# Performance work log

Hardware: AMD Instinct MI355X
Metric: run time of the kernel (lower is better)

The kernel has to match this reference:

```python
import jax, jax.numpy as jnp
import numpy as np

INFINITY = 1000000000000.0
HEADS = 12
HEAD_SIZE = 64


def setup_inputs() -> dict:
    key = jax.random.key(0)
    k1, k2 = jax.random.split(key)
    B, S, H = 8, 512, 1024
    x = jax.random.normal(k1, (B, S, H), dtype=jnp.float32)
    mask = jnp.ones((B, S), dtype=jnp.float32)
    W = jax.random.normal(k2, (H, HEADS * HEAD_SIZE * 2), dtype=jnp.float32) * (1.0 / np.sqrt(H))
    b = jnp.zeros((HEADS * HEAD_SIZE * 2,), dtype=jnp.float32)
    return {"x": x, "mask": mask, "W": W, "b": b}


def _sinusoidal_pos(seq_len, dim, dtype):
    # pos[n, d] interleaved as [sin0, cos0, sin1, cos1, ...]
    position = jnp.arange(seq_len, dtype=dtype)  # (S,)
    indices = jnp.power(jnp.asarray(10000.0, dtype), -2.0 * jnp.arange(dim // 2, dtype=dtype) / dim)
    ang = position[:, None] * indices[None, :]  # (S, d/2)
    pos = jnp.stack([jnp.sin(ang), jnp.cos(ang)], axis=-1).reshape(seq_len, dim)
    return pos


def reference(x, mask, W, b):
    B, S, _ = x.shape
    hs = HEAD_SIZE
    proj = x @ W + b  # (B, S, HEADS*2*hs)
    proj = proj.reshape(B, S, HEADS, 2 * hs)
    qw, kw = proj[..., :hs], proj[..., hs:]  # (B, S, HEADS, hs)

    # RoPE (note: original uses torch .repeat, i.e. TILING, not interleave)
    pos = _sinusoidal_pos(S, hs, x.dtype)  # (S, hs)
    cos_half = pos[None, :, None, 1::2]  # (1, S, 1, hs/2)
    sin_half = pos[None, :, None, ::2]
    cos_pos = jnp.concatenate([cos_half, cos_half], axis=-1)  # tiled -> (1,S,1,hs)
    sin_pos = jnp.concatenate([sin_half, sin_half], axis=-1)

    def rotate(t):
        t2 = jnp.stack([-t[..., 1::2], t[..., ::2]], axis=-1).reshape(t.shape)
        return t * cos_pos + t2 * sin_pos

    qw = rotate(qw)
    kw = rotate(kw)

    logits = jnp.einsum('bmhd,bnhd->bhmn', qw, kw)  # (B, HEADS, S, S)

    # sequence masking on dim 2 (rows) and dim 3 (cols)
    m_row = mask[:, None, :, None]
    m_col = mask[:, None, None, :]
    logits = logits * m_row + (-INFINITY) * (1.0 - m_row)
    logits = logits * m_col + (-INFINITY) * (1.0 - m_col)

    # strictly-lower-triangular mask (exclude end < start)
    tri = jnp.tril(jnp.ones((S, S), dtype=logits.dtype), k=-1)
    logits = logits - tri * INFINITY
    return logits / (hs ** 0.5)
```

## Files before the change

### kernel.cpp

```cpp
#include <hip/hip_runtime.h>
#include <stdint.h>
#include <stddef.h>

#define SS 512
#define HID 1024
#define NHEADS 12
#define HSZ 64
#define NPROJ 1536
#define NEG_INF 1000000000000.0f

typedef __attribute__((ext_vector_type(4))) float f32x4;
typedef __attribute__((ext_vector_type(8))) __bf16 bf16x8;
typedef __attribute__((ext_vector_type(4))) unsigned short us4;

typedef __attribute__((address_space(1))) unsigned char gu8;
typedef __attribute__((address_space(3))) unsigned char lu8;

static __device__ __forceinline__ void gld16(const void* g, void* l) {
  __builtin_amdgcn_global_load_lds((gu8*)(g), (lu8*)(l), 16, 0, 0);
}

static __device__ __forceinline__ unsigned short f2bf(float f) {
  union { float f; unsigned u; } x; x.f = f;
  unsigned r = x.u + 0x7fffu + ((x.u >> 16) & 1u);
  return (unsigned short)(r >> 16);
}

__global__ __launch_bounds__(256) void k_prep(
    const float4* __restrict__ x, const float* __restrict__ W,
    float2* __restrict__ tab, us4* __restrict__ xb, unsigned short* __restrict__ wbt) {
  __shared__ float t[32][33];
  const int bid = blockIdx.x;
  const int tid = threadIdx.x;
  if (bid < 64) {
    int tt = bid * 256 + tid;
    int s = tt >> 5, i = tt & 31;
    float rate = powf(10000.0f, -(float)i / 32.0f);
    float sv, cv;
    sincosf((float)s * rate, &sv, &cv);
    tab[tt] = make_float2(sv, cv);
  } else if (bid < 64 + 4096) {
    int i = (bid - 64) * 256 + tid;
    float4 v = x[i];
    us4 o;
    o[0] = f2bf(v.x); o[1] = f2bf(v.y); o[2] = f2bf(v.z); o[3] = f2bf(v.w);
    xb[i] = o;
  } else {
    int flat = bid - (64 + 4096);
    int n0 = (flat % 48) * 32, k0 = (flat / 48) * 32;
    int tx = tid & 31, ty = tid >> 5;
#pragma unroll
    for (int i = 0; i < 4; ++i)
      t[ty + i * 8][tx] = W[(k0 + ty + i * 8) * NPROJ + n0 + tx];
    __syncthreads();
#pragma unroll
    for (int i = 0; i < 4; ++i)
      wbt[(n0 + ty + i * 8) * HID + (k0 + tx)] = f2bf(t[tx][ty + i * 8]);
  }
}

__global__ __launch_bounds__(256) void k_proj(
    const unsigned short* __restrict__ xb, const unsigned short* __restrict__ wbt,
    const float* __restrict__ bias, const float2* __restrict__ tab,
    unsigned short* __restrict__ qo, unsigned short* __restrict__ ko) {
  __shared__ __align__(16) unsigned short lA[2][128 * 64];
  __shared__ __align__(16) unsigned short lB[2][96 * 64];
  const int tid = threadIdx.x;
  const int lane = tid & 63, w = tid >> 6;
  const int wm = w >> 1, wn = w & 1;
  const int m0 = blockIdx.x * 128, n0 = blockIdx.y * 96;

  const char* aptr[4]; const char* bptr[3];
  int adst[4], bdst[3];
#pragma unroll
  for (int c = 0; c < 4; ++c) {
    int lin = (w * 4 + c) * 1024 + lane * 16;
    int row = lin >> 7, cb = lin & 127;
    aptr[c] = (const char*)(xb + (size_t)(m0 + row) * HID) + (cb ^ ((row & 7) << 4));
    adst[c] = (w * 4 + c) * 1024;
  }
#pragma unroll
  for (int c = 0; c < 3; ++c) {
    int lin = (w * 3 + c) * 1024 + lane * 16;
    int row = lin >> 7, cb = lin & 127;
    bptr[c] = (const char*)(wbt + (size_t)(n0 + row) * HID) + (cb ^ ((row & 7) << 4));
    bdst[c] = (w * 3 + c) * 1024;
  }

  f32x4 acc[3][4];
#pragma unroll
  for (int a = 0; a < 3; ++a)
#pragma unroll
    for (int b = 0; b < 4; ++b)
      acc[a][b] = (f32x4)(0.0f);

#define STAGE(buf, kt)                                                      \
  do {                                                                      \
    _Pragma("unroll") for (int c = 0; c < 4; ++c)                           \
        gld16(aptr[c] + (kt) * 128, (char*)(&lA[(buf)][0]) + adst[c]);      \
    _Pragma("unroll") for (int c = 0; c < 3; ++c)                           \
        gld16(bptr[c] + (kt) * 128, (char*)(&lB[(buf)][0]) + bdst[c]);      \
  } while (0)

  __builtin_amdgcn_sched_barrier(0);
  STAGE(0, 0);

  for (int kt = 0; kt < 16; ++kt) {
    const int cur = kt & 1;
    if (kt < 15) {
      STAGE(cur ^ 1, kt + 1);
      asm volatile("s_waitcnt vmcnt(7)" ::: "memory");
    } else {
      asm volatile("s_waitcnt vmcnt(0)" ::: "memory");
    }
    __builtin_amdgcn_s_barrier();
#pragma unroll
    for (int ks = 0; ks < 2; ++ks) {
      bf16x8 af[3], bf[4];
      const int kb = ks * 64 + (lane >> 4) * 16;
#pragma unroll
      for (int a = 0; a < 3; ++a) {
        int row = wn * 48 + a * 16 + (lane & 15);
        af[a] = *(const bf16x8*)((const char*)(&lB[cur][0]) + row * 128 + (kb ^ ((row & 7) << 4)));
      }
#pragma unroll
      for (int b = 0; b < 4; ++b) {
        int row = wm * 64 + b * 16 + (lane & 15);
        bf[b] = *(const bf16x8*)((const char*)(&lA[cur][0]) + row * 128 + (kb ^ ((row & 7) << 4)));
      }
#pragma unroll
      for (int a = 0; a < 3; ++a)
#pragma unroll
        for (int b = 0; b < 4; ++b)
          acc[a][b] = __builtin_amdgcn_mfma_f32_16x16x32_bf16(af[a], bf[b], acc[a][b], 0, 0, 0);
    }
    asm volatile("s_waitcnt lgkmcnt(0)" ::: "memory");
    __builtin_amdgcn_s_barrier();
  }
#undef STAGE
  __builtin_amdgcn_sched_barrier(0);

#pragma unroll
  for (int a = 0; a < 3; ++a) {
    const int nq = n0 + wn * 48 + a * 16 + (lane >> 4) * 4;
    const float4 bv = *(const float4*)(bias + nq);
    const int d = nq & 63;
    const int h = nq >> 7;
    unsigned short* base = ((nq >> 6) & 1) ? ko : qo;
#pragma unroll
    for (int b = 0; b < 4; ++b) {
      const int mrow = m0 + wm * 64 + b * 16 + (lane & 15);
      const int s = mrow & (SS - 1);
      const int bidx = mrow >> 9;
      const float2* tp = tab + s * 32 + (d & 31);
      const float4 ta = *(const float4*)(tp);
      const float4 tb = *(const float4*)(tp + 2);
      float v0 = acc[a][b][0] + bv.x;
      float v1 = acc[a][b][1] + bv.y;
      float v2 = acc[a][b][2] + bv.z;
      float v3 = acc[a][b][3] + bv.w;
      float o0 = v0 * ta.y - v1 * ta.x;
      float o1 = v1 * ta.w + v0 * ta.z;
      float o2 = v2 * tb.y - v3 * tb.x;
      float o3 = v3 * tb.w + v2 * tb.z;
      us4 pk;
      pk[0] = f2bf(o0); pk[1] = f2bf(o1); pk[2] = f2bf(o2); pk[3] = f2bf(o3);
      *(us4*)(base + ((size_t)(bidx * NHEADS + h) * SS + s) * HSZ + d) = pk;
    }
  }
}

__global__ __launch_bounds__(256) void k_logits(
    const unsigned short* __restrict__ q, const unsigned short* __restrict__ kk,
    const float* __restrict__ mask, float* __restrict__ out) {
  const int tid = threadIdx.x;
  const int lane = tid & 63, w = tid >> 6;
  const int bh = blockIdx.y;
  const int b = bh / NHEADS;
  const int m0 = (blockIdx.x >> 2) * 128, n0 = (blockIdx.x & 3) * 128;
  const char* qbase = (const char*)(q + (size_t)bh * SS * HSZ);
  const char* kbase = (const char*)(kk + (size_t)bh * SS * HSZ);

  int mrow[4], nrow[4];
#pragma unroll
  for (int i = 0; i < 4; ++i) {
    mrow[i] = m0 + (w >> 1) * 64 + i * 16 + (lane & 15);
    nrow[i] = n0 + (w & 1) * 64 + i * 16 + (lane & 15);
  }

  f32x4 acc[4][4];
#pragma unroll
  for (int a = 0; a < 4; ++a)
#pragma unroll
    for (int bb = 0; bb < 4; ++bb)
      acc[a][bb] = (f32x4)(0.0f);

#pragma unroll
  for (int ks = 0; ks < 2; ++ks) {
    const int kboff = ks * 64 + (lane >> 4) * 16;
    bf16x8 kf[4], qf[4];
#pragma unroll
    for (int i = 0; i < 4; ++i)
      kf[i] = *(const bf16x8*)(kbase + (size_t)nrow[i] * 128 + kboff);
#pragma unroll
    for (int i = 0; i < 4; ++i)
      qf[i] = *(const bf16x8*)(qbase + (size_t)mrow[i] * 128 + kboff);
#pragma unroll
    for (int ni = 0; ni < 4; ++ni)
#pragma unroll
      for (int mi = 0; mi < 4; ++mi)
        acc[ni][mi] = __builtin_amdgcn_mfma_f32_16x16x32_bf16(kf[ni], qf[mi], acc[ni][mi], 0, 0, 0);
  }

#pragma unroll
  for (int mi = 0; mi < 4; ++mi) {
    const int m = mrow[mi];
    const float mr = mask[b * SS + m];
    float* orow = out + ((size_t)bh * SS + m) * SS;
#pragma unroll
    for (int ni = 0; ni < 4; ++ni) {
      const int nb = n0 + (w & 1) * 64 + ni * 16 + (lane >> 4) * 4;
      const float4 mc = *(const float4*)(mask + b * SS + nb);
      f32x4 res;
#pragma unroll
      for (int r = 0; r < 4; ++r) {
        float v = acc[ni][mi][r];
        const float mcv = (r == 0) ? mc.x : (r == 1) ? mc.y : (r == 2) ? mc.z : mc.w;
        v = v * mr - NEG_INF * (1.0f - mr);
        v = v * mcv - NEG_INF * (1.0f - mcv);
        if (m > nb + r) v -= NEG_INF;
        res[r] = v * 0.125f;
      }
      *(f32x4*)(orow + nb) = res;
    }
  }
}

extern "C" void kernel_launch(void* const* d_in, const int* in_sizes, int n_in,
                              void* d_out, int out_size, void* d_ws, size_t ws_size,
                              hipStream_t stream) {
  const float* x = (const float*)d_in[0];
  const float* mask = (const float*)d_in[1];
  const float* W = (const float*)d_in[2];
  const float* bias = (const float*)d_in[3];
  float* out = (float*)d_out;

  char* ws = (char*)d_ws;
  float2* tab = (float2*)ws;
  unsigned short* xb = (unsigned short*)(ws + 131072);
  unsigned short* wbt = (unsigned short*)(ws + 131072 + 8388608);
  unsigned short* qo = (unsigned short*)(ws + 131072 + 8388608 + 3145728);
  unsigned short* ko = (unsigned short*)(ws + 131072 + 8388608 + 3145728 + 6291456);

  k_prep<<<dim3(64 + 4096 + 1536), dim3(256), 0, stream>>>(
      (const float4*)x, W, tab, (us4*)xb, wbt);
  k_proj<<<dim3(32, 16), dim3(256), 0, stream>>>(xb, wbt, bias, tab, qo, ko);
  k_logits<<<dim3(16, 96), dim3(256), 0, stream>>>(qo, ko, mask, out);
}
```

Baseline: 59.26 us.

## Fuse prep, projection and logits into one persistent kernel with grid barriers

Merges the three kernels into a single persistent kernel of 512 blocks that loops over the prep, projection and logits work, with atomic-counter grid barriers between phases. This removes two kernel launch boundaries and the drain/ramp gaps between them. In exchange it adds a memset launch, spin-wait barriers, and the risk of deadlock if all 512 blocks are not co-resident (launch bounds request two blocks per CU). Logits work now runs as three iterations per block instead of a wide grid.

After: 181.4 us. 3.06x slower.

```diff
diff --git a/kernel.cpp b/kernel.cpp
--- a/kernel.cpp
+++ b/kernel.cpp
@@ -8,6 +8,7 @@
 #define HSZ 64
 #define NPROJ 1536
 #define NEG_INF 1000000000000.0f
+#define GRID 512
 
 typedef __attribute__((ext_vector_type(4))) float f32x4;
 typedef __attribute__((ext_vector_type(8))) __bf16 bf16x8;
@@ -26,73 +27,95 @@
   return (unsigned short)(r >> 16);
 }
 
-__global__ __launch_bounds__(256) void k_prep(
-    const float4* __restrict__ x, const float* __restrict__ W,
-    float2* __restrict__ tab, us4* __restrict__ xb, unsigned short* __restrict__ wbt) {
-  __shared__ float t[32][33];
+static __device__ __forceinline__ void gbar(unsigned int* cnt) {
+  __syncthreads();
+  if (threadIdx.x == 0) {
+    __threadfence();
+    __hip_atomic_fetch_add(cnt, 1u, __ATOMIC_RELEASE, __HIP_MEMORY_SCOPE_AGENT);
+    while (__hip_atomic_load(cnt, __ATOMIC_RELAXED, __HIP_MEMORY_SCOPE_AGENT) < GRID)
+      __builtin_amdgcn_s_sleep(2);
+    __threadfence();
+  }
+  __syncthreads();
+}
+
+__global__ __launch_bounds__(256, 2) void k_fused(
+    const float4* __restrict__ x, const float* __restrict__ Wg,
+    const float* __restrict__ mask, const float* __restrict__ bias,
+    float2* __restrict__ tab, us4* __restrict__ xb4,
+    unsigned short* __restrict__ wbt,
+    unsigned short* __restrict__ qo, unsigned short* __restrict__ ko,
+    float* __restrict__ out, unsigned int* __restrict__ barcnt) {
+  __shared__ __align__(16) unsigned short smem[2 * 8192 + 2 * 6144];
   const int bid = blockIdx.x;
   const int tid = threadIdx.x;
-  if (bid < 64) {
-    int tt = bid * 256 + tid;
-    int s = tt >> 5, i = tt & 31;
-    float rate = powf(10000.0f, -(float)i / 32.0f);
-    float sv, cv;
-    sincosf((float)s * rate, &sv, &cv);
-    tab[tt] = make_float2(sv, cv);
-  } else if (bid < 64 + 4096) {
-    int i = (bid - 64) * 256 + tid;
-    float4 v = x[i];
-    us4 o;
-    o[0] = f2bf(v.x); o[1] = f2bf(v.y); o[2] = f2bf(v.z); o[3] = f2bf(v.w);
-    xb[i] = o;
-  } else {
-    int flat = bid - (64 + 4096);
-    int n0 = (flat % 48) * 32, k0 = (flat / 48) * 32;
-    int tx = tid & 31, ty = tid >> 5;
-#pragma unroll
-    for (int i = 0; i < 4; ++i)
-      t[ty + i * 8][tx] = W[(k0 + ty + i * 8) * NPROJ + n0 + tx];
-    __syncthreads();
-#pragma unroll
-    for (int i = 0; i < 4; ++i)
-      wbt[(n0 + ty + i * 8) * HID + (k0 + tx)] = f2bf(t[tx][ty + i * 8]);
-  }
-}
-
-__global__ __launch_bounds__(256) void k_proj(
-    const unsigned short* __restrict__ xb, const unsigned short* __restrict__ wbt,
-    const float* __restrict__ bias, const float2* __restrict__ tab,
-    unsigned short* __restrict__ qo, unsigned short* __restrict__ ko) {
-  __shared__ __align__(16) unsigned short lA[2][128 * 64];
-  __shared__ __align__(16) unsigned short lB[2][96 * 64];
-  const int tid = threadIdx.x;
   const int lane = tid & 63, w = tid >> 6;
-  const int wm = w >> 1, wn = w & 1;
-  const int m0 = blockIdx.x * 128, n0 = blockIdx.y * 96;
-
-  const char* aptr[4]; const char* bptr[3];
-  int adst[4], bdst[3];
-#pragma unroll
-  for (int c = 0; c < 4; ++c) {
-    int lin = (w * 4 + c) * 1024 + lane * 16;
-    int row = lin >> 7, cb = lin & 127;
-    aptr[c] = (const char*)(xb + (size_t)(m0 + row) * HID) + (cb ^ ((row & 7) << 4));
-    adst[c] = (w * 4 + c) * 1024;
-  }
-#pragma unroll
-  for (int c = 0; c < 3; ++c) {
-    int lin = (w * 3 + c) * 1024 + lane * 16;
-    int row = lin >> 7, cb = lin & 127;
-    bptr[c] = (const char*)(wbt + (size_t)(n0 + row) * HID) + (cb ^ ((row & 7) << 4));
-    bdst[c] = (w * 3 + c) * 1024;
-  }
-
-  f32x4 acc[3][4];
-#pragma unroll
-  for (int a = 0; a < 3; ++a)
-#pragma unroll
-    for (int b = 0; b < 4; ++b)
-      acc[a][b] = (f32x4)(0.0f);
+
+  {
+    float(*t)[33] = (float(*)[33])smem;
+    const unsigned short* xb2 = (const unsigned short*)xb4;
+    (void)xb2;
+    for (int u = bid; u < 64 + 4096 + 1536; u += GRID) {
+      if (u < 64) {
+        int tt = u * 256 + tid;
+        int s = tt >> 5, i = tt & 31;
+        float rate = powf(10000.0f, -(float)i / 32.0f);
+        float sv, cv;
+        sincosf((float)s * rate, &sv, &cv);
+        tab[tt] = make_float2(sv, cv);
+      } else if (u < 64 + 4096) {
+        int i = (u - 64) * 256 + tid;
+        float4 v = x[i];
+        us4 o;
+        o[0] = f2bf(v.x); o[1] = f2bf(v.y); o[2] = f2bf(v.z); o[3] = f2bf(v.w);
+        xb4[i] = o;
+      } else {
+        int flat = u - (64 + 4096);
+        int n0 = (flat % 48) * 32, k0 = (flat / 48) * 32;
+        int tx = tid & 31, ty = tid >> 5;
+#pragma unroll
+        for (int i = 0; i < 4; ++i)
+          t[ty + i * 8][tx] = Wg[(k0 + ty + i * 8) * NPROJ + n0 + tx];
+        __syncthreads();
+#pragma unroll
+        for (int i = 0; i < 4; ++i)
+          wbt[(n0 + ty + i * 8) * HID + (k0 + tx)] = f2bf(t[tx][ty + i * 8]);
+        __syncthreads();
+      }
+    }
+  }
+  gbar(barcnt + 0);
+
+  {
+    const unsigned short* xb = (const unsigned short*)xb4;
+    unsigned short(*lA)[8192] = (unsigned short(*)[8192])smem;
+    unsigned short(*lB)[6144] = (unsigned short(*)[6144])(smem + 16384);
+    const int wm = w >> 1, wn = w & 1;
+    const int m0 = (bid & 31) * 128, n0 = (bid >> 5) * 96;
+
+    const char* aptr[4]; const char* bptr[3];
+    int adst[4], bdst[3];
+#pragma unroll
+    for (int c = 0; c < 4; ++c) {
+      int lin = (w * 4 + c) * 1024 + lane * 16;
+      int row = lin >> 7, cb = lin & 127;
+      aptr[c] = (const char*)(xb + (size_t)(m0 + row) * HID) + (cb ^ ((row & 7) << 4));
+      adst[c] = (w * 4 + c) * 1024;
+    }
+#pragma unroll
+    for (int c = 0; c < 3; ++c) {
+      int lin = (w * 3 + c) * 1024 + lane * 16;
+      int row = lin >> 7, cb = lin & 127;
+      bptr[c] = (const char*)(wbt + (size_t)(n0 + row) * HID) + (cb ^ ((row & 7) << 4));
+      bdst[c] = (w * 3 + c) * 1024;
+    }
+
+    f32x4 acc[3][4];
+#pragma unroll
+    for (int a = 0; a < 3; ++a)
+#pragma unroll
+      for (int b = 0; b < 4; ++b)
+        acc[a][b] = (f32x4)(0.0f);
 
 #define STAGE(buf, kt)                                                      \
   do {                                                                      \
@@ -102,136 +125,135 @@
         gld16(bptr[c] + (kt) * 128, (char*)(&lB[(buf)][0]) + bdst[c]);      \
   } while (0)
 
-  __builtin_amdgcn_sched_barrier(0);
-  STAGE(0, 0);
-
-  for (int kt = 0; kt < 16; ++kt) {
-    const int cur = kt & 1;
-    if (kt < 15) {
-      STAGE(cur ^ 1, kt + 1);
-      asm volatile("s_waitcnt vmcnt(7)" ::: "memory");
-    } else {
-      asm volatile("s_waitcnt vmcnt(0)" ::: "memory");
-    }
-    __builtin_amdgcn_s_barrier();
+    __builtin_amdgcn_sched_barrier(0);
+    STAGE(0, 0);
+
+    for (int kt = 0; kt < 16; ++kt) {
+      const int cur = kt & 1;
+      if (kt < 15) {
+        STAGE(cur ^ 1, kt + 1);
+        asm volatile("s_waitcnt vmcnt(7)" ::: "memory");
+      } else {
+        asm volatile("s_waitcnt vmcnt(0)" ::: "memory");
+      }
+      __builtin_amdgcn_s_barrier();
+#pragma unroll
+      for (int ks = 0; ks < 2; ++ks) {
+        bf16x8 af[3], bf[4];
+        const int kb = ks * 64 + (lane >> 4) * 16;
+#pragma unroll
+        for (int a = 0; a < 3; ++a) {
+          int row = wn * 48 + a * 16 + (lane & 15);
+          af[a] = *(const bf16x8*)((const char*)(&lB[cur][0]) + row * 128 + (kb ^ ((row & 7) << 4)));
+        }
+#pragma unroll
+        for (int b = 0; b < 4; ++b) {
+          int row = wm * 64 + b * 16 + (lane & 15);
+          bf[b] = *(const bf16x8*)((const char*)(&lA[cur][0]) + row * 128 + (kb ^ ((row & 7) << 4)));
+        }
+#pragma unroll
+        for (int a = 0; a < 3; ++a)
+#pragma unroll
+          for (int b = 0; b < 4; ++b)
+            acc[a][b] = __builtin_amdgcn_mfma_f32_16x16x32_bf16(af[a], bf[b], acc[a][b], 0, 0, 0);
+      }
+      asm volatile("s_waitcnt lgkmcnt(0)" ::: "memory");
+      __builtin_amdgcn_s_barrier();
+    }
+#undef STAGE
+    __builtin_amdgcn_sched_barrier(0);
+
+#pragma unroll
+    for (int a = 0; a < 3; ++a) {
+      const int nq = n0 + wn * 48 + a * 16 + (lane >> 4) * 4;
+      const float4 bv = *(const float4*)(bias + nq);
+      const int d = nq & 63;
+      const int h = nq >> 7;
+      unsigned short* base = ((nq >> 6) & 1) ? ko : qo;
+#pragma unroll
+      for (int b = 0; b < 4; ++b) {
+        const int mrow = m0 + wm * 64 + b * 16 + (lane & 15);
+        const int s = mrow & (SS - 1);
+        const int bidx = mrow >> 9;
+        const float2* tp = tab + s * 32 + (d & 31);
+        const float4 ta = *(const float4*)(tp);
+        const float4 tb = *(const float4*)(tp + 2);
+        float v0 = acc[a][b][0] + bv.x;
+        float v1 = acc[a][b][1] + bv.y;
+        float v2 = acc[a][b][2] + bv.z;
+        float v3 = acc[a][b][3] + bv.w;
+        float o0 = v0 * ta.y - v1 * ta.x;
+        float o1 = v1 * ta.w + v0 * ta.z;
+        float o2 = v2 * tb.y - v3 * tb.x;
+        float o3 = v3 * tb.w + v2 * tb.z;
+        us4 pk;
+        pk[0] = f2bf(o0); pk[1] = f2bf(o1); pk[2] = f2bf(o2); pk[3] = f2bf(o3);
+        *(us4*)(base + ((size_t)(bidx * NHEADS + h) * SS + s) * HSZ + d) = pk;
+      }
+    }
+  }
+  gbar(barcnt + 1);
+
+  for (int tt = bid; tt < 1536; tt += GRID) {
+    const int bx = tt & 15;
+    const int bh = tt >> 4;
+    const int b = bh / NHEADS;
+    const int m0 = (bx >> 2) * 128, n0 = (bx & 3) * 128;
+    const char* qbase = (const char*)(qo + (size_t)bh * SS * HSZ);
+    const char* kbase = (const char*)(ko + (size_t)bh * SS * HSZ);
+
+    int mrow[4], nrow[4];
+#pragma unroll
+    for (int i = 0; i < 4; ++i) {
+      mrow[i] = m0 + (w >> 1) * 64 + i * 16 + (lane & 15);
+      nrow[i] = n0 + (w & 1) * 64 + i * 16 + (lane & 15);
+    }
+
+    f32x4 acc[4][4];
+#pragma unroll
+    for (int a = 0; a < 4; ++a)
+#pragma unroll
+      for (int bb = 0; bb < 4; ++bb)
+        acc[a][bb] = (f32x4)(0.0f);
+
 #pragma unroll
     for (int ks = 0; ks < 2; ++ks) {
-      bf16x8 af[3], bf[4];
-      const int kb = ks * 64 + (lane >> 4) * 16;
-#pragma unroll
-      for (int a = 0; a < 3; ++a) {
-        int row = wn * 48 + a * 16 + (lane & 15);
-        af[a] = *(const bf16x8*)((const char*)(&lB[cur][0]) + row * 128 + (kb ^ ((row & 7) << 4)));
-      }
-#pragma unroll
-      for (int b = 0; b < 4; ++b) {
-        int row = wm * 64 + b * 16 + (lane & 15);
-        bf[b] = *(const bf16x8*)((const char*)(&lA[cur][0]) + row * 128 + (kb ^ ((row & 7) << 4)));
-      }
-#pragma unroll
-      for (int a = 0; a < 3; ++a)
-#pragma unroll
-        for (int b = 0; b < 4; ++b)
-          acc[a][b] = __builtin_amdgcn_mfma_f32_16x16x32_bf16(af[a], bf[b], acc[a][b], 0, 0, 0);
-    }
-    asm volatile("s_waitcnt lgkmcnt(0)" ::: "memory");
-    __builtin_amdgcn_s_barrier();
-  }
-#undef STAGE
-  __builtin_amdgcn_sched_barrier(0);
-
-#pragma unroll
-  for (int a = 0; a < 3; ++a) {
-    const int nq = n0 + wn * 48 + a * 16 + (lane >> 4) * 4;
-    const float4 bv = *(const float4*)(bias + nq);
-    const int d = nq & 63;
-    const int h = nq >> 7;
-    unsigned short* base = ((nq >> 6) & 1) ? ko : qo;
-#pragma unroll
-    for (int b = 0; b < 4; ++b) {
-      const int mrow = m0 + wm * 64 + b * 16 + (lane & 15);
-      const int s = mrow & (SS - 1);
-      const int bidx = mrow >> 9;
-      const float2* tp = tab + s * 32 + (d & 31);
-      const float4 ta = *(const float4*)(tp);
-      const float4 tb = *(const float4*)(tp + 2);
-      float v0 = acc[a][b][0] + bv.x;
-      float v1 = acc[a][b][1] + bv.y;
-      float v2 = acc[a][b][2] + bv.z;
-      float v3 = acc[a][b][3] + bv.w;
-      float o0 = v0 * ta.y - v1 * ta.x;
-      float o1 = v1 * ta.w + v0 * ta.z;
-      float o2 = v2 * tb.y - v3 * tb.x;
-      float o3 = v3 * tb.w + v2 * tb.z;
-      us4 pk;
-      pk[0] = f2bf(o0); pk[1] = f2bf(o1); pk[2] = f2bf(o2); pk[3] = f2bf(o3);
-      *(us4*)(base + ((size_t)(bidx * NHEADS + h) * SS + s) * HSZ + d) = pk;
-    }
-  }
-}
-
-__global__ __launch_bounds__(256) void k_logits(
-    const unsigned short* __restrict__ q, const unsigned short* __restrict__ kk,
-    const float* __restrict__ mask, float* __restrict__ out) {
-  const int tid = threadIdx.x;
-  const int lane = tid & 63, w = tid >> 6;
-  const int bh = blockIdx.y;
-  const int b = bh / NHEADS;
-  const int m0 = (blockIdx.x >> 2) * 128, n0 = (blockIdx.x & 3) * 128;
-  const char* qbase = (const char*)(q + (size_t)bh * SS * HSZ);
-  const char* kbase = (const char*)(kk + (size_t)bh * SS * HSZ);
-
-  int mrow[4], nrow[4];
-#pragma unroll
-  for (int i = 0; i < 4; ++i) {
-    mrow[i] = m0 + (w >> 1) * 64 + i * 16 + (lane & 15);
-    nrow[i] = n0 + (w & 1) * 64 + i * 16 + (lane & 15);
-  }
-
-  f32x4 acc[4][4];
-#pragma unroll
-  for (int a = 0; a < 4; ++a)
-#pragma unroll
-    for (int bb = 0; bb < 4; ++bb)
-      acc[a][bb] = (f32x4)(0.0f);
-
-#pragma unroll
-  for (int ks = 0; ks < 2; ++ks) {
-    const int kboff = ks * 64 + (lane >> 4) * 16;
-    bf16x8 kf[4], qf[4];
-#pragma unroll
-    for (int i = 0; i < 4; ++i)
-      kf[i] = *(const bf16x8*)(kbase + (size_t)nrow[i] * 128 + kboff);
-#pragma unroll
-    for (int i = 0; i < 4; ++i)
-      qf[i] = *(const bf16x8*)(qbase + (size_t)mrow[i] * 128 + kboff);
-#pragma unroll
-    for (int ni = 0; ni < 4; ++ni)
-#pragma unroll
-      for (int mi = 0; mi < 4; ++mi)
-        acc[ni][mi] = __builtin_amdgcn_mfma_f32_16x16x32_bf16(kf[ni], qf[mi], acc[ni][mi], 0, 0, 0);
-  }
-
-#pragma unroll
-  for (int mi = 0; mi < 4; ++mi) {
-    const int m = mrow[mi];
-    const float mr = mask[b * SS + m];
-    float* orow = out + ((size_t)bh * SS + m) * SS;
-#pragma unroll
-    for (int ni = 0; ni < 4; ++ni) {
-      const int nb = n0 + (w & 1) * 64 + ni * 16 + (lane >> 4) * 4;
-      const float4 mc = *(const float4*)(mask + b * SS + nb);
-      f32x4 res;
-#pragma unroll
-      for (int r = 0; r < 4; ++r) {
-        float v = acc[ni][mi][r];
-        const float mcv = (r == 0) ? mc.x : (r == 1) ? mc.y : (r == 2) ? mc.z : mc.w;
-        v = v * mr - NEG_INF * (1.0f - mr);
-        v = v * mcv - NEG_INF * (1.0f - mcv);
-        if (m > nb + r) v -= NEG_INF;
-        res[r] = v * 0.125f;
-      }
-      *(f32x4*)(orow + nb) = res;
+      const int kboff = ks * 64 + (lane >> 4) * 16;
+      bf16x8 kf[4], qf[4];
+#pragma unroll
+      for (int i = 0; i < 4; ++i)
+        kf[i] = *(const bf16x8*)(kbase + (size_t)nrow[i] * 128 + kboff);
+#pragma unroll
+      for (int i = 0; i < 4; ++i)
+        qf[i] = *(const bf16x8*)(qbase + (size_t)mrow[i] * 128 + kboff);
+#pragma unroll
+      for (int ni = 0; ni < 4; ++ni)
+#pragma unroll
+        for (int mi = 0; mi < 4; ++mi)
+          acc[ni][mi] = __builtin_amdgcn_mfma_f32_16x16x32_bf16(kf[ni], qf[mi], acc[ni][mi], 0, 0, 0);
+    }
+
+#pragma unroll
+    for (int mi = 0; mi < 4; ++mi) {
+      const int m = mrow[mi];
+      const float mr = mask[b * SS + m];
+      float* orow = out + ((size_t)bh * SS + m) * SS;
+#pragma unroll
+      for (int ni = 0; ni < 4; ++ni) {
+        const int nb = n0 + (w & 1) * 64 + ni * 16 + (lane >> 4) * 4;
+        const float4 mc = *(const float4*)(mask + b * SS + nb);
+        f32x4 res;
+#pragma unroll
+        for (int r = 0; r < 4; ++r) {
+          float v = acc[ni][mi][r];
+          const float mcv = (r == 0) ? mc.x : (r == 1) ? mc.y : (r == 2) ? mc.z : mc.w;
+          v = v * mr - NEG_INF * (1.0f - mr);
+          v = v * mcv - NEG_INF * (1.0f - mcv);
+          if (m > nb + r) v -= NEG_INF;
+          res[r] = v * 0.125f;
+        }
+        *(f32x4*)(orow + nb) = res;
+      }
     }
   }
 }
@@ -251,9 +273,9 @@
   unsigned short* wbt = (unsigned short*)(ws + 131072 + 8388608);
   unsigned short* qo = (unsigned short*)(ws + 131072 + 8388608 + 3145728);
   unsigned short* ko = (unsigned short*)(ws + 131072 + 8388608 + 3145728 + 6291456);
-
-  k_prep<<<dim3(64 + 4096 + 1536), dim3(256), 0, stream>>>(
-      (const float4*)x, W, tab, (us4*)xb, wbt);
-  k_proj<<<dim3(32, 16), dim3(256), 0, stream>>>(xb, wbt, bias, tab, qo, ko);
-  k_logits<<<dim3(16, 96), dim3(256), 0, stream>>>(qo, ko, mask, out);
-}
+  unsigned int* barcnt = (unsigned int*)(ws + 32 * 1024 * 1024);
+
+  hipMemsetAsync(barcnt, 0, 8, stream);
+  k_fused<<<dim3(GRID), dim3(256), 0, stream>>>(
+      (const float4*)x, W, mask, bias, tab, (us4*)xb, wbt, qo, ko, out, barcnt);
+}
```

## Skip MFMA for fully masked lower-triangular tiles and reuse Q fragments across N tiles

Applied to the files above, without the earlier changes.

The logits kernel moves to a 1D grid in which each block covers one 128-row M tile and two 128-column N tiles. The Q fragments are loaded once per block and reused for both N tiles. Tiles lying entirely below the diagonal skip the MFMA work and write the mask-derived constant directly. This relies on the -1e12 offset absorbing the small dot product in fp32. The constant-store path uses an odd column indexing that writes overlapping and out-of-tile addresses, which adds redundant store traffic. Dead index code was also left in the prep kernel.

After: 65.64 us. 1.11x slower.

```diff
diff --git a/kernel.cpp b/kernel.cpp
--- a/kernel.cpp
+++ b/kernel.cpp
@@ -40,7 +40,12 @@
     sincosf((float)s * rate, &sv, &cv);
     tab[tt] = make_float2(sv, cv);
   } else if (bid < 64 + 4096) {
-    int i = (bid - 64) * 256 + tid;
+    int bidc = bid - 64;
+    int xcd = bidc & 7, idx = bidc >> 3;
+    int ttile = xcd + 8 * (idx & 3);
+    int r = ttile * 128 + (idx >> 2);
+    int i = r * 4 + tid / 64 * 64 + (tid & 63);
+    i = r * 256 + tid;
     float4 v = x[i];
     us4 o;
     o[0] = f2bf(v.x); o[1] = f2bf(v.y); o[2] = f2bf(v.z); o[3] = f2bf(v.w);
@@ -175,63 +180,129 @@
     const float* __restrict__ mask, float* __restrict__ out) {
   const int tid = threadIdx.x;
   const int lane = tid & 63, w = tid >> 6;
-  const int bh = blockIdx.y;
-  const int b = bh / NHEADS;
-  const int m0 = (blockIdx.x >> 2) * 128, n0 = (blockIdx.x & 3) * 128;
+  const int bid = blockIdx.x;
+  const int rowtile = bid & 31;
+  const int b = rowtile >> 2, mt = rowtile & 3;
+  const int rest = bid >> 5;
+  const int h = rest % NHEADS;
+  const int nh = rest / NHEADS;
+  const int bh = b * NHEADS + h;
+  const int m0 = mt * 128;
   const char* qbase = (const char*)(q + (size_t)bh * SS * HSZ);
   const char* kbase = (const char*)(kk + (size_t)bh * SS * HSZ);
-
-  int mrow[4], nrow[4];
-#pragma unroll
-  for (int i = 0; i < 4; ++i) {
-    mrow[i] = m0 + (w >> 1) * 64 + i * 16 + (lane & 15);
-    nrow[i] = n0 + (w & 1) * 64 + i * 16 + (lane & 15);
-  }
-
-  f32x4 acc[4][4];
-#pragma unroll
-  for (int a = 0; a < 4; ++a)
-#pragma unroll
-    for (int bb = 0; bb < 4; ++bb)
-      acc[a][bb] = (f32x4)(0.0f);
-
+  const int wm = w >> 1, wn = w & 1;
+
+  int mrow[4];
+#pragma unroll
+  for (int i = 0; i < 4; ++i) mrow[i] = m0 + wm * 64 + i * 16 + (lane & 15);
+
+  float mr[4][4];
+#pragma unroll
+  for (int mi = 0; mi < 4; ++mi) {
+    const int mq = m0 + wm * 64 + mi * 16 + (lane >> 4) * 4;
+#pragma unroll
+    for (int r = 0; r < 4; ++r) mr[mi][r] = mask[b * SS + mq + r];
+  }
+
+  bf16x8 qf[2][4];
 #pragma unroll
   for (int ks = 0; ks < 2; ++ks) {
     const int kboff = ks * 64 + (lane >> 4) * 16;
-    bf16x8 kf[4], qf[4];
 #pragma unroll
     for (int i = 0; i < 4; ++i)
-      kf[i] = *(const bf16x8*)(kbase + (size_t)nrow[i] * 128 + kboff);
-#pragma unroll
-    for (int i = 0; i < 4; ++i)
-      qf[i] = *(const bf16x8*)(qbase + (size_t)mrow[i] * 128 + kboff);
-#pragma unroll
-    for (int ni = 0; ni < 4; ++ni)
-#pragma unroll
-      for (int mi = 0; mi < 4; ++mi)
-        acc[ni][mi] = __builtin_amdgcn_mfma_f32_16x16x32_bf16(kf[ni], qf[mi], acc[ni][mi], 0, 0, 0);
-  }
-
-#pragma unroll
-  for (int mi = 0; mi < 4; ++mi) {
-    const int m = mrow[mi];
-    const float mr = mask[b * SS + m];
-    float* orow = out + ((size_t)bh * SS + m) * SS;
-#pragma unroll
-    for (int ni = 0; ni < 4; ++ni) {
-      const int nb = n0 + (w & 1) * 64 + ni * 16 + (lane >> 4) * 4;
-      const float4 mc = *(const float4*)(mask + b * SS + nb);
-      f32x4 res;
-#pragma unroll
-      for (int r = 0; r < 4; ++r) {
-        float v = acc[ni][mi][r];
-        const float mcv = (r == 0) ? mc.x : (r == 1) ? mc.y : (r == 2) ? mc.z : mc.w;
-        v = v * mr - NEG_INF * (1.0f - mr);
-        v = v * mcv - NEG_INF * (1.0f - mcv);
-        if (m > nb + r) v -= NEG_INF;
-        res[r] = v * 0.125f;
-      }
-      *(f32x4*)(orow + nb) = res;
+      qf[ks][i] = *(const bf16x8*)(qbase + (size_t)mrow[i] * 128 + kboff);
+  }
+
+#pragma unroll
+  for (int nt2 = 0; nt2 < 2; ++nt2) {
+    const int n0 = (nh * 2 + nt2) * 128;
+    if (n0 + 128 <= m0) {
+#pragma unroll
+      for (int mi = 0; mi < 4; ++mi) {
+#pragma unroll
+        for (int r = 0; r < 4; ++r) {
+          const int m = m0 + wm * 64 + mi * 16 + (lane >> 4) * 4 + r;
+          const float mrv = mr[mi][r];
+          float* orow = out + ((size_t)bh * SS + m) * SS;
+          const float base_v = -NEG_INF * (1.0f - mrv);
+#pragma unroll
+          for (int ni = 0; ni < 4; ++ni) {
+            const int nb = n0 + wn * 64 + ni * 16 + (lane & 15) * 0 + (lane >> 4) * 0;
+            (void)nb;
+          }
+        }
+      }
+#pragma unroll
+      for (int mi = 0; mi < 4; ++mi) {
+#pragma unroll
+        for (int r = 0; r < 4; ++r) {
+          const int m = m0 + wm * 64 + mi * 16 + (lane >> 4) * 4 + r;
+          const float mrv = mr[mi][r];
+          float* orow = out + ((size_t)bh * SS + m) * SS;
+#pragma unroll
+          for (int ni = 0; ni < 4; ++ni) {
+            const int nb = n0 + wn * 64 + ni * 16 + (lane & 15) * 4;
+            const float4 mc = *(const float4*)(mask + b * SS + nb);
+            f32x4 res;
+#pragma unroll
+            for (int rr = 0; rr < 4; ++rr) {
+              const float mcv = (rr == 0) ? mc.x : (rr == 1) ? mc.y : (rr == 2) ? mc.z : mc.w;
+              float v = -NEG_INF * (1.0f - mrv);
+              v = v * mcv - NEG_INF * (1.0f - mcv);
+              v -= NEG_INF;
+              res[rr] = v * 0.125f;
+            }
+            *(f32x4*)(orow + nb) = res;
+          }
+        }
+      }
+      continue;
+    }
+
+    f32x4 acc[4][4];
+#pragma unroll
+    for (int a = 0; a < 4; ++a)
+#pragma unroll
+      for (int bb = 0; bb < 4; ++bb)
+        acc[a][bb] = (f32x4)(0.0f);
+
+#pragma unroll
+    for (int ks = 0; ks < 2; ++ks) {
+      const int kboff = ks * 64 + (lane >> 4) * 16;
+      bf16x8 kf[4];
+#pragma unroll
+      for (int i = 0; i < 4; ++i) {
+        const int nrow = n0 + wn * 64 + i * 16 + (lane & 15);
+        kf[i] = *(const bf16x8*)(kbase + (size_t)nrow * 128 + kboff);
+      }
+#pragma unroll
+      for (int ni = 0; ni < 4; ++ni)
+#pragma unroll
+        for (int mi = 0; mi < 4; ++mi)
+          acc[ni][mi] = __builtin_amdgcn_mfma_f32_16x16x32_bf16(kf[ni], qf[ks][mi], acc[ni][mi], 0, 0, 0);
+    }
+
+#pragma unroll
+    for (int mi = 0; mi < 4; ++mi) {
+      const int m = mrow[mi];
+      const float mrv = mask[b * SS + m];
+      float* orow = out + ((size_t)bh * SS + m) * SS;
+#pragma unroll
+      for (int ni = 0; ni < 4; ++ni) {
+        const int nb = n0 + wn * 64 + ni * 16 + (lane >> 4) * 4;
+        const float4 mc = *(const float4*)(mask + b * SS + nb);
+        f32x4 res;
+#pragma unroll
+        for (int r = 0; r < 4; ++r) {
+          float v = acc[ni][mi][r];
+          const float mcv = (r == 0) ? mc.x : (r == 1) ? mc.y : (r == 2) ? mc.z : mc.w;
+          v = v * mrv - NEG_INF * (1.0f - mrv);
+          v = v * mcv - NEG_INF * (1.0f - mcv);
+          if (m > nb + r) v -= NEG_INF;
+          res[r] = v * 0.125f;
+        }
+        *(f32x4*)(orow + nb) = res;
+      }
     }
   }
 }
@@ -255,5 +326,5 @@
   k_prep<<<dim3(64 + 4096 + 1536), dim3(256), 0, stream>>>(
       (const float4*)x, W, tab, (us4*)xb, wbt);
   k_proj<<<dim3(32, 16), dim3(256), 0, stream>>>(xb, wbt, bias, tab, qo, ko);
-  k_logits<<<dim3(16, 96), dim3(256), 0, stream>>>(qo, ko, mask, out);
-}
+  k_logits<<<dim3(768), dim3(256), 0, stream>>>(qo, ko, mask, out);
+}
```
